# Optimization experiments

Measured on AMD Instinct MI355X. Metric: run time of the kernel, lower is better.

## Reference

```python
import jax, jax.numpy as jnp
import numpy as np

HIDDEN = 100
INPUT = 4


def setup_inputs() -> dict:
    key = jax.random.key(0)
    k_x, k_len, k_wi, k_wh, k_bi, k_bh = jax.random.split(key, 6)
    N, T = 4096, 256
    x = jax.random.normal(k_x, (N, T, INPUT), dtype=jnp.float32)
    lengths = jax.random.randint(k_len, (N,), 1, T + 1, dtype=jnp.int32)
    # PyTorch LSTM params: weight_ih [4H, I], weight_hh [4H, H] (uniform(-0.05,0.05)
    # per the module's init), biases [4H]. Gate order: i, f, g, o.
    s = 1.0 / np.sqrt(HIDDEN)
    w_ih = jax.random.uniform(k_wi, (4 * HIDDEN, INPUT), minval=-s, maxval=s, dtype=jnp.float32)
    w_hh = jax.random.uniform(k_wh, (4 * HIDDEN, HIDDEN), minval=-0.05, maxval=0.05, dtype=jnp.float32)
    b_ih = jax.random.uniform(k_bi, (4 * HIDDEN,), minval=-s, maxval=s, dtype=jnp.float32)
    b_hh = jax.random.uniform(k_bh, (4 * HIDDEN,), minval=-s, maxval=s, dtype=jnp.float32)
    return {"long_ttf": x, "w_ih": w_ih, "w_hh": w_hh, "b_ih": b_ih, "b_hh": b_hh, "lengths": lengths}


def _lstm_last(x, w_ih, w_hh, b_ih, b_hh, lengths):
    # x: [N, T, I]; returns h at step (length-1) per sequence -> [N, H]
    N, T, _ = x.shape
    xs = jnp.swapaxes(x, 0, 1)  # [T, N, I]
    # mask[t, n] = t < lengths[n]; freeze (h, c) once a sequence has ended,
    # so the final carry equals the output at its last valid step.
    mask = (jnp.arange(T, dtype=jnp.int32)[:, None] < lengths[None, :])[:, :, None]  # [T, N, 1]
    bias = b_ih + b_hh

    def step(carry, inp):
        h, c = carry
        xt, m = inp
        gates = xt @ w_ih.T + h @ w_hh.T + bias  # [N, 4H]
        i = jax.nn.sigmoid(gates[:, 0 * HIDDEN:1 * HIDDEN])
        f = jax.nn.sigmoid(gates[:, 1 * HIDDEN:2 * HIDDEN])
        g = jnp.tanh(gates[:, 2 * HIDDEN:3 * HIDDEN])
        o = jax.nn.sigmoid(gates[:, 3 * HIDDEN:4 * HIDDEN])
        c_new = f * c + i * g
        h_new = o * jnp.tanh(c_new)
        h = jnp.where(m, h_new, h)
        c = jnp.where(m, c_new, c)
        return (h, c), None

    h0 = jnp.zeros((N, HIDDEN), dtype=x.dtype)
    c0 = jnp.zeros((N, HIDDEN), dtype=x.dtype)
    (h, _), _ = jax.lax.scan(step, (h0, c0), (xs, mask))
    return h


def reference(long_ttf, w_ih, w_hh, b_ih, b_hh, lengths):
    return _lstm_last(long_ttf, w_ih, w_hh, b_ih, b_hh, lengths)
```

## Files before the change

### kernel.cpp

```cpp
#include <hip/hip_runtime.h>

#define HID    100
#define INP    4
#define TMAX   256
#define SB     16
#define ULD    136
#define NTH    1024
#define NTILES 25

typedef _Float16 half8  __attribute__((ext_vector_type(8)));
typedef _Float16 half2v __attribute__((ext_vector_type(2)));
typedef float    f32x4  __attribute__((ext_vector_type(4)));

#define L2E  1.442695040888963f
#define L2E2 2.885390081777927f

__device__ __forceinline__ float fexp2(float x) { return __builtin_amdgcn_exp2f(x); }
__device__ __forceinline__ float frcp(float x)  { return __builtin_amdgcn_rcpf(x); }

__device__ __forceinline__ int pos_for(int n, int g) {
    int base = 25 * g;
    int e = base + (base & 1);
    if (n < 9)   return e + 2 * n;
    if (n >= 16) return e + 2 * (n - 16) + 1;
    if (base & 1) return (n == 9) ? base : base + 19 + (n - 10);
    return base + 18 + (n - 9);
}

__global__ __launch_bounds__(NTH) void lstm_persist(
    const float* __restrict__ xg,
    const float* __restrict__ w_ih,
    const float* __restrict__ w_hh,
    const float* __restrict__ b_ih,
    const float* __restrict__ b_hh,
    const int*   __restrict__ lens,
    float* __restrict__ out)
{
    __shared__ _Float16 u_lds[2][SB * ULD];
    __shared__ int len_s[SB];
    __shared__ int maxlen_s;

    const int tid  = threadIdx.x;
    const int wave = tid >> 6;
    const int lane = tid & 63;
    const int l15  = lane & 15;
    const int l4   = lane >> 4;
    const int seq0 = blockIdx.x * SB;

    if (tid < SB) len_s[tid] = lens[seq0 + tid];
    {
        _Float16* u0 = &u_lds[0][0];
        for (int i = tid; i < 2 * SB * ULD; i += NTH) {
            int col = i % ULD;
            u0[i] = (col == (HID + INP)) ? (_Float16)1.f : (_Float16)0.f;
        }
    }

    half8 afrag[2][4];
    int   tn[2];
    tn[0] = wave;
    tn[1] = (wave + 16 < NTILES) ? wave + 16 : NTILES;
    #pragma unroll
    for (int i = 0; i < 2; ++i) {
        int n = tn[i];
        if (n < NTILES) {
            int ty   = l15 & 3;
            int unit = pos_for(n, l15 >> 2);
            int grow = ty * HID + unit;
            float scale = (ty == 2) ? L2E2 : -L2E;
            #pragma unroll
            for (int c = 0; c < 4; ++c) {
                half8 v;
                #pragma unroll
                for (int j = 0; j < 8; ++j) {
                    int k = c * 32 + l4 * 8 + j;
                    float w;
                    if (k < HID)             w = w_hh[grow * HID + k];
                    else if (k < HID + INP)  w = w_ih[grow * INP + (k - HID)];
                    else if (k == HID + INP) w = b_ih[grow] + b_hh[grow];
                    else                     w = 0.f;
                    v[j] = (_Float16)(scale * w);
                }
                afrag[i][c] = v;
            }
        }
    }

    __syncthreads();
    if (tid == 0) {
        int m = 0;
        for (int s = 0; s < SB; ++s) m = m > len_s[s] ? m : len_s[s];
        maxlen_s = m;
    }

    float xv1 = 0.f, xv2 = 0.f;
    const float* xs = nullptr;
    if (tid >= NTH - 64) {
        int idx = tid - (NTH - 64);
        int s = idx >> 2, ch = idx & 3;
        xs = xg + (size_t)(seq0 + s) * TMAX * INP + ch;
        u_lds[0][s * ULD + HID + ch] = (_Float16)xs[0];
        xv1 = xs[INP];
        xv2 = xs[2 * INP];
    }
    float creg[2] = {};
    __syncthreads();

    if (wave & 1) __builtin_amdgcn_s_setprio(1);

    const bool has2 = (wave < 9);
    const int  pos0 = pos_for(tn[0], l4);
    const int  pos1 = has2 ? pos_for(tn[1], l4) : 0;

    const int maxlen = maxlen_s;
    const int mylen  = len_s[l15];
    const _Float16* ub0 = &u_lds[0][l15 * ULD + l4 * 8];
    const _Float16* ub1 = &u_lds[1][l15 * ULD + l4 * 8];

    for (int t = 0; t < maxlen; ++t) {
        const _Float16* ub = (t & 1) ? ub1 : ub0;
        _Float16* ubn = (t & 1) ? &u_lds[0][0] : &u_lds[1][0];

        half8 bfr[4];
        #pragma unroll
        for (int c = 0; c < 4; ++c)
            bfr[c] = *(const half8*)(ub + c * 32);

        if (tid >= NTH - 64) {
            int idx = tid - (NTH - 64);
            int s = idx >> 2, ch = idx & 3;
            ubn[s * ULD + HID + ch] = (_Float16)xv1;
            xv1 = xv2;
            int tt = t + 3;
            xv2 = (tt < TMAX) ? xs[(size_t)tt * INP] : 0.f;
        }

        f32x4 acc0 = {0.f, 0.f, 0.f, 0.f};
        #pragma unroll
        for (int c = 0; c < 4; ++c)
            acc0 = __builtin_amdgcn_mfma_f32_16x16x32_f16(afrag[0][c], bfr[c], acc0, 0, 0, 0);
        f32x4 acc1 = {0.f, 0.f, 0.f, 0.f};
        if (has2) {
            #pragma unroll
            for (int c = 0; c < 4; ++c)
                acc1 = __builtin_amdgcn_mfma_f32_16x16x32_f16(afrag[1][c], bfr[c], acc1, 0, 0, 0);
        }

        if (t < mylen) {
            float e_i = fexp2(acc0[0]);
            float e_f = fexp2(acc0[1]);
            float e_g = fexp2(acc0[2]);
            float e_o = fexp2(acc0[3]);
            float tg  = 1.f + e_g;
            float df  = 1.f + e_f;
            float d1  = __builtin_fmaf(e_i, tg, tg);
            float r12 = frcp(d1 * df);
            float r1  = df * r12;
            float fm  = d1 * r12;
            float ig  = __builtin_fmaf(e_g, r1, -r1);
            float cn  = __builtin_fmaf(fm, creg[0], ig);
            float e_c = fexp2(fminf(L2E2 * cn, 60.f));
            float t3  = 1.f + e_c;
            float d3  = __builtin_fmaf(e_o, t3, t3);
            float r3  = frcp(d3);
            float hn0 = __builtin_fmaf(e_c, r3, -r3);
            creg[0] = cn;

            float hn1 = 0.f;
            if (has2) {
                float f_i = fexp2(acc1[0]);
                float f_f = fexp2(acc1[1]);
                float f_g = fexp2(acc1[2]);
                float f_o = fexp2(acc1[3]);
                float ug  = 1.f + f_g;
                float uf  = 1.f + f_f;
                float u1  = __builtin_fmaf(f_i, ug, ug);
                float s12 = frcp(u1 * uf);
                float s1  = uf * s12;
                float um  = u1 * s12;
                float jg  = __builtin_fmaf(f_g, s1, -s1);
                float dn  = __builtin_fmaf(um, creg[1], jg);
                float f_c = fexp2(fminf(L2E2 * dn, 60.f));
                float u3  = 1.f + f_c;
                float w3  = __builtin_fmaf(f_o, u3, u3);
                float s3  = frcp(w3);
                hn1 = __builtin_fmaf(f_c, s3, -s3);
                creg[1] = dn;
            }

            if (has2) {
                half2v pk = {(_Float16)hn0, (_Float16)hn1};
                *(half2v*)(ubn + l15 * ULD + pos0) = pk;
            } else {
                ubn[l15 * ULD + pos0] = (_Float16)hn0;
            }
            if (t == mylen - 1) {
                out[(size_t)(seq0 + l15) * HID + pos0] = hn0;
                if (has2) out[(size_t)(seq0 + l15) * HID + pos1] = hn1;
            }
        }
        asm volatile("s_waitcnt lgkmcnt(0)" ::: "memory");
        __builtin_amdgcn_s_barrier();
    }
}

extern "C" void kernel_launch(void* const* d_in, const int* in_sizes, int n_in,
                              void* d_out, int out_size, void* d_ws, size_t ws_size,
                              hipStream_t stream) {
    const float* xg   = (const float*)d_in[0];
    const float* w_ih = (const float*)d_in[1];
    const float* w_hh = (const float*)d_in[2];
    const float* b_ih = (const float*)d_in[3];
    const float* b_hh = (const float*)d_in[4];
    const int*   lens = (const int*)d_in[5];
    float* out = (float*)d_out;
    const int N = in_sizes[5];
    lstm_persist<<<dim3(N / SB), NTH, 0, stream>>>(xg, w_ih, w_hh, b_ih, b_hh, lens, out);
}
```

Baseline: 178.4 us.

## Simplify gate math, unroll ping-pong loop, drop paired h-unit permutation

Rewrites the cell update so c_new comes from one shared reciprocal of a combined numerator and denominator, which removes a reciprocal and several multiplies per unit. The time loop is unrolled by two so the double-buffer pointers become constants, and the x-prefetch store is moved after the MFMAs so it no longer sits between the LDS reads and the matrix ops. The pos_for permutation that let each lane write two adjacent fp16 values together is dropped in favour of natural unit indexing with two separate scalar LDS stores. The changed cell algebra may slightly alter rounding.

```diff
diff --git a/kernel.cpp b/kernel.cpp
--- a/kernel.cpp
+++ b/kernel.cpp
@@ -8,24 +8,14 @@
 #define NTH    1024
 #define NTILES 25
 
-typedef _Float16 half8  __attribute__((ext_vector_type(8)));
-typedef _Float16 half2v __attribute__((ext_vector_type(2)));
-typedef float    f32x4  __attribute__((ext_vector_type(4)));
+typedef _Float16 half8 __attribute__((ext_vector_type(8)));
+typedef float    f32x4 __attribute__((ext_vector_type(4)));
 
 #define L2E  1.442695040888963f
 #define L2E2 2.885390081777927f
 
 __device__ __forceinline__ float fexp2(float x) { return __builtin_amdgcn_exp2f(x); }
 __device__ __forceinline__ float frcp(float x)  { return __builtin_amdgcn_rcpf(x); }
-
-__device__ __forceinline__ int pos_for(int n, int g) {
-    int base = 25 * g;
-    int e = base + (base & 1);
-    if (n < 9)   return e + 2 * n;
-    if (n >= 16) return e + 2 * (n - 16) + 1;
-    if (base & 1) return (n == 9) ? base : base + 19 + (n - 10);
-    return base + 18 + (n - 9);
-}
 
 __global__ __launch_bounds__(NTH) void lstm_persist(
     const float* __restrict__ xg,
@@ -65,7 +55,7 @@
         int n = tn[i];
         if (n < NTILES) {
             int ty   = l15 & 3;
-            int unit = pos_for(n, l15 >> 2);
+            int unit = 25 * (l15 >> 2) + n;
             int grow = ty * HID + unit;
             float scale = (ty == 2) ? L2E2 : -L2E;
             #pragma unroll
@@ -108,32 +98,19 @@
 
     if (wave & 1) __builtin_amdgcn_s_setprio(1);
 
-    const bool has2 = (wave < 9);
-    const int  pos0 = pos_for(tn[0], l4);
-    const int  pos1 = has2 ? pos_for(tn[1], l4) : 0;
-
-    const int maxlen = maxlen_s;
-    const int mylen  = len_s[l15];
-    const _Float16* ub0 = &u_lds[0][l15 * ULD + l4 * 8];
-    const _Float16* ub1 = &u_lds[1][l15 * ULD + l4 * 8];
-
-    for (int t = 0; t < maxlen; ++t) {
-        const _Float16* ub = (t & 1) ? ub1 : ub0;
-        _Float16* ubn = (t & 1) ? &u_lds[0][0] : &u_lds[1][0];
-
+    const bool has2  = (tn[1] < NTILES);
+    const int  maxlen = maxlen_s;
+    const int  mylen  = len_s[l15];
+    const _Float16* ubr0 = &u_lds[0][l15 * ULD + l4 * 8];
+    const _Float16* ubr1 = &u_lds[1][l15 * ULD + l4 * 8];
+    _Float16* ubw0 = &u_lds[0][0];
+    _Float16* ubw1 = &u_lds[1][0];
+
+    auto step = [&](const _Float16* ubr, _Float16* ubw, int t) {
         half8 bfr[4];
         #pragma unroll
         for (int c = 0; c < 4; ++c)
-            bfr[c] = *(const half8*)(ub + c * 32);
-
-        if (tid >= NTH - 64) {
-            int idx = tid - (NTH - 64);
-            int s = idx >> 2, ch = idx & 3;
-            ubn[s * ULD + HID + ch] = (_Float16)xv1;
-            xv1 = xv2;
-            int tt = t + 3;
-            xv2 = (tt < TMAX) ? xs[(size_t)tt * INP] : 0.f;
-        }
+            bfr[c] = *(const half8*)(ubr + c * 32);
 
         f32x4 acc0 = {0.f, 0.f, 0.f, 0.f};
         #pragma unroll
@@ -146,6 +123,15 @@
                 acc1 = __builtin_amdgcn_mfma_f32_16x16x32_f16(afrag[1][c], bfr[c], acc1, 0, 0, 0);
         }
 
+        if (tid >= NTH - 64) {
+            int idx = tid - (NTH - 64);
+            int s = idx >> 2, ch = idx & 3;
+            ubw[s * ULD + HID + ch] = (_Float16)xv1;
+            xv1 = xv2;
+            int tt = t + 3;
+            xv2 = (tt < TMAX) ? xs[(size_t)tt * INP] : 0.f;
+        }
+
         if (t < mylen) {
             float e_i = fexp2(acc0[0]);
             float e_f = fexp2(acc0[1]);
@@ -153,20 +139,19 @@
             float e_o = fexp2(acc0[3]);
             float tg  = 1.f + e_g;
             float df  = 1.f + e_f;
-            float d1  = __builtin_fmaf(e_i, tg, tg);
-            float r12 = frcp(d1 * df);
-            float r1  = df * r12;
-            float fm  = d1 * r12;
-            float ig  = __builtin_fmaf(e_g, r1, -r1);
-            float cn  = __builtin_fmaf(fm, creg[0], ig);
+            float A   = __builtin_fmaf(e_i, tg, tg);
+            float P   = __builtin_fmaf(e_g, df, -df);
+            float num = __builtin_fmaf(creg[0], A, P);
+            float cn  = num * frcp(A * df);
             float e_c = fexp2(fminf(L2E2 * cn, 60.f));
             float t3  = 1.f + e_c;
             float d3  = __builtin_fmaf(e_o, t3, t3);
             float r3  = frcp(d3);
             float hn0 = __builtin_fmaf(e_c, r3, -r3);
             creg[0] = cn;
-
-            float hn1 = 0.f;
+            int unit0 = 25 * l4 + tn[0];
+            ubw[l15 * ULD + unit0] = (_Float16)hn0;
+
             if (has2) {
                 float f_i = fexp2(acc1[0]);
                 float f_f = fexp2(acc1[1]);
@@ -174,33 +159,36 @@
                 float f_o = fexp2(acc1[3]);
                 float ug  = 1.f + f_g;
                 float uf  = 1.f + f_f;
-                float u1  = __builtin_fmaf(f_i, ug, ug);
-                float s12 = frcp(u1 * uf);
-                float s1  = uf * s12;
-                float um  = u1 * s12;
-                float jg  = __builtin_fmaf(f_g, s1, -s1);
-                float dn  = __builtin_fmaf(um, creg[1], jg);
+                float B   = __builtin_fmaf(f_i, ug, ug);
+                float Q   = __builtin_fmaf(f_g, uf, -uf);
+                float nm2 = __builtin_fmaf(creg[1], B, Q);
+                float dn  = nm2 * frcp(B * uf);
                 float f_c = fexp2(fminf(L2E2 * dn, 60.f));
                 float u3  = 1.f + f_c;
                 float w3  = __builtin_fmaf(f_o, u3, u3);
                 float s3  = frcp(w3);
-                hn1 = __builtin_fmaf(f_c, s3, -s3);
+                float hn1 = __builtin_fmaf(f_c, s3, -s3);
                 creg[1] = dn;
-            }
-
-            if (has2) {
-                half2v pk = {(_Float16)hn0, (_Float16)hn1};
-                *(half2v*)(ubn + l15 * ULD + pos0) = pk;
-            } else {
-                ubn[l15 * ULD + pos0] = (_Float16)hn0;
-            }
-            if (t == mylen - 1) {
-                out[(size_t)(seq0 + l15) * HID + pos0] = hn0;
-                if (has2) out[(size_t)(seq0 + l15) * HID + pos1] = hn1;
+                int unit1 = 25 * l4 + tn[1];
+                ubw[l15 * ULD + unit1] = (_Float16)hn1;
+                if (t == mylen - 1) {
+                    out[(size_t)(seq0 + l15) * HID + unit0] = hn0;
+                    out[(size_t)(seq0 + l15) * HID + unit1] = hn1;
+                }
+            } else if (t == mylen - 1) {
+                out[(size_t)(seq0 + l15) * HID + unit0] = hn0;
             }
         }
         asm volatile("s_waitcnt lgkmcnt(0)" ::: "memory");
         __builtin_amdgcn_s_barrier();
+    };
+
+    int t = 0;
+    while (true) {
+        step(ubr0, ubw1, t);
+        if (++t >= maxlen) break;
+        step(ubr1, ubw0, t);
+        if (++t >= maxlen) break;
     }
 }
 
```

After: 175.4 us. No clear change (-1.7%).
